# Kernel tuning notes

Measured on AMD Instinct MI355X. Metric: run time of the kernel, lower is better.

Reference implementation:

```python
import jax, jax.numpy as jnp
import numpy as np
import math

N_NODES = 16384
N_GRAPHS = 512
E2 = 65536
E3 = 393216
EMB = 300
SCH = 128
NG = 50
CUTOFF = 10.0
NL_GIN = 5
NL_SCH = 6
NTASK = 12


def _ssp(x):
    # ShiftedSoftplus used by SchNet
    return jax.nn.softplus(x) - math.log(2.0)


def _seg(x, ids, n):
    return jax.ops.segment_sum(x, ids, num_segments=n)


def _forward(x2d, edge_index_2d, edge_attr_2d, batch, z, pos, edge_index_3d,
             atom_emb1, atom_emb2, vn_init,
             gin_W1, gin_b1, gin_W2, gin_b2, gin_bond1, gin_bond2, gin_gamma, gin_beta,
             vn_W1, vn_b1, vn_W2, vn_b2,
             sch_emb, s_mW1, s_mb1, s_mW2, s_mb2, s_lin1W, s_lin2W, s_lin2b, s_linW, s_linb,
             p2W, p2b, p3W, p3b, gW1, gb1, gW2, gb2, cW1, cb1, cW2, cb2):
    counts = jnp.maximum(_seg(jnp.ones((N_NODES,), jnp.float32), batch, N_GRAPHS), 1.0)[:, None]
    # ---------- GIN (2D) encoder with virtual node (OGB-style, eval mode: dropout off, BN uses running stats 0/1) ----------
    src2, dst2 = edge_index_2d[0], edge_index_2d[1]
    h = atom_emb1[x2d[:, 0]] + atom_emb2[x2d[:, 1]]              # [N, 300]
    vn = jnp.broadcast_to(vn_init, (N_GRAPHS, EMB))
    for l in range(NL_GIN):
        h_in = h + vn[batch]
        eemb = gin_bond1[l][edge_attr_2d[:, 0]] + gin_bond2[l][edge_attr_2d[:, 1]]
        msg = jax.nn.relu(h_in[src2] + eemb)                     # [E2, 300]
        agg = _seg(msg, dst2, N_NODES)
        t = jax.nn.relu((h_in + agg) @ gin_W1[l] + gin_b1[l]) @ gin_W2[l] + gin_b2[l]
        t = t * gin_gamma[l] + gin_beta[l]                       # eval-mode BatchNorm
        if l < NL_GIN - 1:
            t = jax.nn.relu(t)
            vn_tmp = _seg(t, batch, N_GRAPHS) + vn
            vn = jax.nn.relu(jax.nn.relu(vn_tmp @ vn_W1[l] + vn_b1[l]) @ vn_W2[l] + vn_b2[l])
        h = t
    h2d = _seg(h, batch, N_GRAPHS) / counts                      # global_mean_pool
    # ---------- SchNet (3D) encoder: interaction layers only, residual additions ----------
    src3, dst3 = edge_index_3d[0], edge_index_3d[1]
    diff = pos[dst3] - pos[src3]
    d = jnp.sqrt(jnp.sum(diff * diff, axis=-1))                  # edge_weight [E3]; no self loops -> d > 0
    offsets = jnp.linspace(0.0, CUTOFF, NG)
    coeff = -0.5 / (offsets[1] - offsets[0]) ** 2
    rbf = jnp.exp(coeff * (d[:, None] - offsets) ** 2)           # GaussianSmearing [E3, 50]
    C = 0.5 * (jnp.cos(d * math.pi / CUTOFF) + 1.0)              # cosine cutoff
    hs = sch_emb[z]                                              # [N, 128]
    for l in range(NL_SCH):
        Wf = (_ssp(rbf @ s_mW1[l] + s_mb1[l]) @ s_mW2[l] + s_mb2[l]) * C[:, None]  # filter net [E3, 128]
        x1 = hs @ s_lin1W[l]                                     # CFConv lin1 (no bias)
        agg = _seg(x1[src3] * Wf, dst3, N_NODES)                 # continuous-filter conv
        x2 = agg @ s_lin2W[l] + s_lin2b[l]                       # CFConv lin2
        hs = hs + (_ssp(x2) @ s_linW[l] + s_linb[l])             # block act+lin, residual
    h3d = _seg(hs, batch, N_GRAPHS) / counts
    # ---------- gated fusion + classifier (dropout off in eval) ----------
    h2p = h2d @ p2W + p2b
    h3p = h3d @ p3W + p3b
    g = jax.nn.sigmoid(jax.nn.relu(jnp.concatenate([h2p, h3p], axis=1) @ gW1 + gb1) @ gW2 + gb2)  # [B, 1]
    hf = g * h2p + (1.0 - g) * h3p
    return jax.nn.relu(hf @ cW1 + cb1) @ cW2 + cb2               # [N_GRAPHS, NTASK]


def setup_inputs() -> dict:
    key = jax.random.key(0)
    ks = jax.random.split(key, 40)
    def r(i, shape, s=0.02):
        return jax.random.normal(ks[i], shape, dtype=jnp.float32) * s
    x2d = jax.random.randint(ks[0], (N_NODES, 2), 0, 3)
    src2 = jax.random.randint(ks[1], (E2,), 0, N_NODES)
    dst2 = (src2 + jax.random.randint(ks[2], (E2,), 1, N_NODES)) % N_NODES  # no self loops
    edge_index_2d = jnp.stack([src2, dst2])
    edge_attr_2d = jax.random.randint(ks[3], (E2, 2), 0, 3)
    batch = jnp.sort(jax.random.randint(ks[4], (N_NODES,), 0, N_GRAPHS))
    z = jax.random.randint(ks[5], (N_NODES,), 0, 100)
    pos = jax.random.normal(ks[6], (N_NODES, 3), dtype=jnp.float32) * 2.0
    src3 = jax.random.randint(ks[7], (E3,), 0, N_NODES)
    dst3 = (src3 + jax.random.randint(ks[8], (E3,), 1, N_NODES)) % N_NODES
    edge_index_3d = jnp.stack([src3, dst3])
    return dict(
        x2d=x2d, edge_index_2d=edge_index_2d, edge_attr_2d=edge_attr_2d, batch=batch,
        z=z, pos=pos, edge_index_3d=edge_index_3d,
        atom_emb1=r(9, (120, EMB)), atom_emb2=r(10, (3, EMB)),
        vn_init=jnp.zeros((EMB,), jnp.float32),
        gin_W1=r(11, (NL_GIN, EMB, 2 * EMB)), gin_b1=jnp.zeros((NL_GIN, 2 * EMB), jnp.float32),
        gin_W2=r(12, (NL_GIN, 2 * EMB, EMB)), gin_b2=jnp.zeros((NL_GIN, EMB), jnp.float32),
        gin_bond1=r(13, (NL_GIN, 6, EMB)), gin_bond2=r(14, (NL_GIN, 3, EMB)),
        gin_gamma=jnp.ones((NL_GIN, EMB), jnp.float32), gin_beta=jnp.zeros((NL_GIN, EMB), jnp.float32),
        vn_W1=r(15, (NL_GIN - 1, EMB, 2 * EMB)), vn_b1=jnp.zeros((NL_GIN - 1, 2 * EMB), jnp.float32),
        vn_W2=r(16, (NL_GIN - 1, 2 * EMB, EMB)), vn_b2=jnp.zeros((NL_GIN - 1, EMB), jnp.float32),
        sch_emb=r(17, (100, SCH), 0.1),
        s_mW1=r(18, (NL_SCH, NG, SCH), 0.1), s_mb1=jnp.zeros((NL_SCH, SCH), jnp.float32),
        s_mW2=r(19, (NL_SCH, SCH, SCH), 0.1), s_mb2=jnp.zeros((NL_SCH, SCH), jnp.float32),
        s_lin1W=r(20, (NL_SCH, SCH, SCH), 0.1),
        s_lin2W=r(21, (NL_SCH, SCH, SCH), 0.1), s_lin2b=jnp.zeros((NL_SCH, SCH), jnp.float32),
        s_linW=r(22, (NL_SCH, SCH, SCH), 0.1), s_linb=jnp.zeros((NL_SCH, SCH), jnp.float32),
        p2W=r(23, (EMB, EMB)), p2b=jnp.zeros((EMB,), jnp.float32),
        p3W=r(24, (SCH, EMB)), p3b=jnp.zeros((EMB,), jnp.float32),
        gW1=r(25, (2 * EMB, 128)), gb1=jnp.zeros((128,), jnp.float32),
        gW2=r(26, (128, 1)), gb2=jnp.zeros((1,), jnp.float32),
        cW1=r(27, (EMB, EMB // 2)), cb1=jnp.zeros((EMB // 2,), jnp.float32),
        cW2=r(28, (EMB // 2, NTASK)), cb2=jnp.zeros((NTASK,), jnp.float32),
    )


def reference(x2d, edge_index_2d, edge_attr_2d, batch, z, pos, edge_index_3d,
              atom_emb1, atom_emb2, vn_init,
              gin_W1, gin_b1, gin_W2, gin_b2, gin_bond1, gin_bond2, gin_gamma, gin_beta,
              vn_W1, vn_b1, vn_W2, vn_b2,
              sch_emb, s_mW1, s_mb1, s_mW2, s_mb2, s_lin1W, s_lin2W, s_lin2b, s_linW, s_linb,
              p2W, p2b, p3W, p3b, gW1, gb1, gW2, gb2, cW1, cb1, cW2, cb2):
    return _forward(x2d, edge_index_2d, edge_attr_2d, batch, z, pos, edge_index_3d,
                    atom_emb1, atom_emb2, vn_init,
                    gin_W1, gin_b1, gin_W2, gin_b2, gin_bond1, gin_bond2, gin_gamma, gin_beta,
                    vn_W1, vn_b1, vn_W2, vn_b2,
                    sch_emb, s_mW1, s_mb1, s_mW2, s_mb2, s_lin1W, s_lin2W, s_lin2b, s_linW, s_linb,
                    p2W, p2b, p3W, p3b, gW1, gb1, gW2, gb2, cW1, cb1, cW2, cb2)
```

## Files before the change

### kernel.cpp

```cpp
#include <hip/hip_runtime.h>
#include <hip/hip_bf16.h>
#include <math.h>

#define NN 16384
#define NG 512
#define NE2 65536
#define NE3 393216
#define DEMB 300
#define DSCH 128
#define NRBF 50
#define NTAB 5120
#define TROWS 5121
#define DMAX 25.0f

typedef __attribute__((ext_vector_type(8))) short bf16x8;
typedef __attribute__((ext_vector_type(4))) float f32x4;

__device__ __forceinline__ float sspf(float x) {
  float sp = log1pf(expf(-fabsf(x))) + fmaxf(x, 0.f);
  return sp - 0.69314718055994530942f;
}

__device__ __forceinline__ short f2b(float f) {
  union { float f; unsigned u; } v;
  v.f = f;
  unsigned r = v.u + 0x7FFF + ((v.u >> 16) & 1);
  return (short)(r >> 16);
}

__device__ __forceinline__ float b2f(unsigned short b) {
  union { unsigned u; float f; } v;
  v.u = ((unsigned)b) << 16;
  return v.f;
}


__global__ void k_hist3(const int* __restrict__ ei2, const int* __restrict__ ei3,
                        const int* __restrict__ batch, int* __restrict__ cnt2,
                        int* __restrict__ cnt3, int* __restrict__ cntg) {
  int i = blockIdx.x * blockDim.x + threadIdx.x;
  if (i < NE2) {
    atomicAdd(&cnt2[ei2[NE2 + i]], 1);
  } else if (i < NE2 + NE3) {
    atomicAdd(&cnt3[ei3[NE3 + (i - NE2)]], 1);
  } else if (i < NE2 + NE3 + NN) {
    atomicAdd(&cntg[batch[i - NE2 - NE3]], 1);
  }
}

__global__ __launch_bounds__(1024) void k_scan3(const int* __restrict__ c0, int* __restrict__ o0,
                                                int n0, const int* __restrict__ c1,
                                                int* __restrict__ o1, int n1,
                                                const int* __restrict__ c2, int* __restrict__ o2,
                                                int n2) {
  const int* cnt = (blockIdx.x == 0) ? c0 : (blockIdx.x == 1) ? c1 : c2;
  int* off = (blockIdx.x == 0) ? o0 : (blockIdx.x == 1) ? o1 : o2;
  int n = (blockIdx.x == 0) ? n0 : (blockIdx.x == 1) ? n1 : n2;
  __shared__ int part[1024];
  int tid = threadIdx.x;
  int per = (n + 1023) / 1024;
  int base = tid * per;
  int sum = 0;
  for (int i = 0; i < per; ++i) {
    int idx = base + i;
    if (idx < n) sum += cnt[idx];
  }
  part[tid] = sum;
  __syncthreads();
  for (int d = 1; d < 1024; d <<= 1) {
    int v = (tid >= d) ? part[tid - d] : 0;
    __syncthreads();
    part[tid] += v;
    __syncthreads();
  }
  int run = (tid == 0) ? 0 : part[tid - 1];
  for (int i = 0; i < per; ++i) {
    int idx = base + i;
    if (idx < n) {
      off[idx] = run;
      run += cnt[idx];
    }
  }
  if (tid == 0) off[n] = part[1023];
}

__global__ void k_scatterB(const int* __restrict__ ei2, const int* __restrict__ ea2,
                           const int* __restrict__ batch, const int* __restrict__ off2,
                           int* __restrict__ cur2, int* __restrict__ s2s, int* __restrict__ ec2s,
                           int* __restrict__ b2s, const int* __restrict__ ei3,
                           const float* __restrict__ pos, const int* __restrict__ off3,
                           int* __restrict__ cur3, int* __restrict__ s3s, int* __restrict__ id3s,
                           float* __restrict__ fr3s) {
  int i = blockIdx.x * blockDim.x + threadIdx.x;
  if (i < NE2) {
    int e = i;
    int s = ei2[e], d = ei2[NE2 + e];
    int p = atomicAdd(&cur2[d], 1);
    int j = off2[d] + p;
    s2s[j] = s;
    ec2s[j] = ea2[2 * e] * 4 + ea2[2 * e + 1];
    b2s[j] = batch[s];
  } else if (i < NE2 + NE3) {
    int e = i - NE2;
    int s = ei3[e], d = ei3[NE3 + e];
    float dx = pos[3 * d] - pos[3 * s];
    float dy = pos[3 * d + 1] - pos[3 * s + 1];
    float dz = pos[3 * d + 2] - pos[3 * s + 2];
    float dist = sqrtf(dx * dx + dy * dy + dz * dz);
    float u = fminf(dist * ((float)NTAB / DMAX), (float)NTAB - 0.001f);
    int idx = (int)u;
    int p = atomicAdd(&cur3[d], 1);
    int j = off3[d] + p;
    s3s[j] = s;
    id3s[j] = idx;
    fr3s[j] = u - (float)idx;
  }
}


__global__ void k_init_gin(const int* __restrict__ x2d, const float* __restrict__ e1,
                           const float* __restrict__ e2, short* __restrict__ hb,
                           const float* __restrict__ vni, float* __restrict__ vn,
                           short* __restrict__ vnb) {
  int i = blockIdx.x * blockDim.x + threadIdx.x;
  if (i < NN * DEMB) {
    int n = i / DEMB, c = i - n * DEMB;
    hb[i] = f2b(e1[x2d[2 * n] * DEMB + c] + e2[x2d[2 * n + 1] * DEMB + c]);
  } else if (i < NN * DEMB + NG * DEMB) {
    int j = i - NN * DEMB;
    float v = vni[j % DEMB];
    vn[j] = v;
    vnb[j] = f2b(v);
  }
}

__global__ void k_init_sch(float* __restrict__ rbs, float* __restrict__ Cs,
                           const int* __restrict__ z, const float* __restrict__ emb,
                           float* __restrict__ hs, short* __restrict__ hsb) {
  int i = blockIdx.x * blockDim.x + threadIdx.x;
  if (i < TROWS * NRBF) {
    int j = i / NRBF, k = i - j * NRBF;
    float dj = (float)j * (DMAX / (float)NTAB);
    const float step = 10.0f / 49.0f;
    const float coeff = -0.5f / (step * step);
    float t = dj - (float)k * step;
    rbs[i] = expf(coeff * t * t);
    if (k == 0) Cs[j] = 0.5f * (cosf(dj * (3.14159265358979323846f / 10.0f)) + 1.0f);
  } else if (i < TROWS * NRBF + NN * DSCH) {
    int j = i - TROWS * NRBF;
    float v = emb[z[j >> 7] * DSCH + (j & 127)];
    hs[j] = v;
    hsb[j] = f2b(v);
  }
}

__global__ __launch_bounds__(256) void k_head4(
    const float* __restrict__ h2d, const float* __restrict__ h3d, const float* __restrict__ p2W,
    const float* __restrict__ p2b, const float* __restrict__ p3W, const float* __restrict__ p3b,
    const float* __restrict__ gW1, const float* __restrict__ gb1, const float* __restrict__ gW2,
    const float* __restrict__ gb2, const float* __restrict__ cW1, const float* __restrict__ cb1,
    const float* __restrict__ cW2, const float* __restrict__ cb2, float* __restrict__ out) {
  __shared__ float sx[DEMB], sy[DSCH], h2p[DEMB], h3p[DEMB], ghl[DSCH], c1l[150];
  __shared__ float pa[2][128], pb[2][128];
  __shared__ float gshare;
  int g = blockIdx.x, tid = threadIdx.x;
  int half = tid >> 7, o7 = tid & 127;
  for (int i = tid; i < DEMB; i += 256) sx[i] = h2d[(size_t)g * DEMB + i];
  if (tid < DSCH) sy[tid] = h3d[(size_t)g * DSCH + tid];
  __syncthreads();
  for (int ob = 0; ob < DEMB; ob += 128) {
    int o = ob + o7;
    float a = 0.f, b = 0.f;
    if (o < DEMB) {
      for (int k = half * 150; k < half * 150 + 150; ++k) a = fmaf(sx[k], p2W[k * 300 + o], a);
      for (int k = half * 64; k < half * 64 + 64; ++k) b = fmaf(sy[k], p3W[k * 300 + o], b);
    }
    pa[half][o7] = a;
    pb[half][o7] = b;
    __syncthreads();
    if (half == 0 && o < DEMB) {
      h2p[o] = pa[0][o7] + pa[1][o7] + p2b[o];
      h3p[o] = pb[0][o7] + pb[1][o7] + p3b[o];
    }
    __syncthreads();
  }
  {
    float a = 0.f;
    if (half == 0) {
      for (int k = 0; k < 300; ++k) a = fmaf(h2p[k], gW1[k * 128 + o7], a);
    } else {
      for (int k = 0; k < 300; ++k) a = fmaf(h3p[k], gW1[(300 + k) * 128 + o7], a);
    }
    pa[half][o7] = a;
    __syncthreads();
    if (half == 0) ghl[o7] = fmaxf(pa[0][o7] + pa[1][o7] + gb1[o7], 0.f);
    __syncthreads();
  }
  if (tid < 128) pa[0][tid] = ghl[tid] * gW2[tid];
  __syncthreads();
  for (int s = 64; s > 0; s >>= 1) {
    if (tid < s) pa[0][tid] += pa[0][tid + s];
    __syncthreads();
  }
  if (tid == 0) gshare = 1.0f / (1.0f + expf(-(pa[0][0] + gb2[0])));
  __syncthreads();
  float gg = gshare;
  for (int i = tid; i < DEMB; i += 256) sx[i] = gg * h2p[i] + (1.0f - gg) * h3p[i];
  __syncthreads();
  for (int ob = 0; ob < 150; ob += 128) {
    int o = ob + o7;
    float a = 0.f;
    if (o < 150) {
      for (int k = half * 150; k < half * 150 + 150; ++k) a = fmaf(sx[k], cW1[k * 150 + o], a);
    }
    pa[half][o7] = a;
    __syncthreads();
    if (half == 0 && o < 150) c1l[o] = fmaxf(pa[0][o7] + pa[1][o7] + cb1[o], 0.f);
    __syncthreads();
  }
  if (tid < 12) {
    float a = cb2[tid];
    for (int k = 0; k < 150; ++k) a = fmaf(c1l[k], cW2[k * 12 + tid], a);
    out[(size_t)g * 12 + tid] = a;
  }
}


__global__ __launch_bounds__(256) void k_gin_gather4(
    const short* __restrict__ hb, const short* __restrict__ vnb, const int* __restrict__ batch,
    const int* __restrict__ off2, const int* __restrict__ s2s, const int* __restrict__ ec2s,
    const int* __restrict__ b2s, const float* __restrict__ bond1,
    const float* __restrict__ bond2, short* __restrict__ aggb) {
  __shared__ float sb[9 * DEMB];
  int tid = threadIdx.x;
  for (int i = tid; i < 6 * DEMB; i += 256) sb[i] = bond1[i];
  for (int i = tid; i < 3 * DEMB; i += 256) sb[6 * DEMB + i] = bond2[i];
  __syncthreads();
  int d = blockIdx.x * 4 + (tid >> 6);
  int lane = tid & 63;
  int j0 = off2[d], j1 = off2[d + 1];
  const unsigned short* hd = (const unsigned short*)hb + (size_t)d * DEMB;
  const unsigned short* vd = (const unsigned short*)vnb + (size_t)batch[d] * DEMB;
  float acc[5];
#pragma unroll
  for (int q = 0; q < 5; ++q) {
    int col = lane + 64 * q;
    acc[q] = (col < DEMB) ? b2f(hd[col]) + b2f(vd[col]) : 0.f;
  }
  for (int j = j0; j < j1; ++j) {
    int s = s2s[j], ec = ec2s[j], bs = b2s[j];
    const unsigned short* hr = (const unsigned short*)hb + (size_t)s * DEMB;
    const unsigned short* vr = (const unsigned short*)vnb + (size_t)bs * DEMB;
    const float* b1 = sb + (ec >> 2) * DEMB;
    const float* b2 = sb + 6 * DEMB + (ec & 3) * DEMB;
#pragma unroll
    for (int q = 0; q < 5; ++q) {
      int col = lane + 64 * q;
      if (col < DEMB) acc[q] += fmaxf(b2f(hr[col]) + b2f(vr[col]) + b1[col] + b2[col], 0.f);
    }
  }
  short* outr = aggb + (size_t)d * 320;
#pragma unroll
  for (int q = 0; q < 5; ++q) {
    int col = lane + 64 * q;
    outr[col] = (col < DEMB) ? f2b(acc[q]) : (short)0;
  }
}

__global__ __launch_bounds__(256) void k_conv_gather4(
    const short* __restrict__ ftabb, const short* __restrict__ x1b, const int* __restrict__ off3,
    const int* __restrict__ s3s, const int* __restrict__ id3s, const float* __restrict__ fr3s,
    short* __restrict__ agg3b) {
  int tid = threadIdx.x;
  int d = blockIdx.x * 4 + (tid >> 6);
  int lane = tid & 63;
  int j0 = off3[d], j1 = off3[d + 1];
  float a0 = 0.f, a1 = 0.f;
  for (int j = j0; j < j1; ++j) {
    int s = s3s[j], idx = id3s[j];
    float fr = fr3s[j];
    unsigned t0 = ((const unsigned*)(ftabb + (size_t)idx * 128))[lane];
    unsigned t1 = ((const unsigned*)(ftabb + (size_t)(idx + 1) * 128))[lane];
    unsigned xv = ((const unsigned*)(x1b + (size_t)s * 128))[lane];
    float t0a = b2f((unsigned short)(t0 & 0xFFFF)), t0b = b2f((unsigned short)(t0 >> 16));
    float t1a = b2f((unsigned short)(t1 & 0xFFFF)), t1b = b2f((unsigned short)(t1 >> 16));
    a0 += (t0a + fr * (t1a - t0a)) * b2f((unsigned short)(xv & 0xFFFF));
    a1 += (t0b + fr * (t1b - t0b)) * b2f((unsigned short)(xv >> 16));
  }
  unsigned pack = ((unsigned)(unsigned short)f2b(a1) << 16) | (unsigned short)f2b(a0);
  ((unsigned*)(agg3b + (size_t)d * 128))[lane] = pack;
}

__global__ __launch_bounds__(256) void k_poolb300(const short* __restrict__ xb,
                                                  const int* __restrict__ goff,
                                                  float* __restrict__ out) {
  int g = blockIdx.x * 4 + (threadIdx.x >> 6);
  int lane = threadIdx.x & 63;
  if (g >= NG) return;
  int r0 = goff[g], r1 = goff[g + 1];
  float acc[5] = {};
  for (int r = r0; r < r1; ++r) {
    const unsigned short* row = (const unsigned short*)xb + (size_t)r * DEMB;
#pragma unroll
    for (int q = 0; q < 5; ++q) {
      int col = lane + 64 * q;
      if (col < DEMB) acc[q] += b2f(row[col]);
    }
  }
  float s = 1.0f / fmaxf((float)(r1 - r0), 1.0f);
#pragma unroll
  for (int q = 0; q < 5; ++q) {
    int col = lane + 64 * q;
    if (col < DEMB) out[(size_t)g * DEMB + col] = acc[q] * s;
  }
}

__global__ __launch_bounds__(256) void k_poolb128(const short* __restrict__ xb,
                                                  const int* __restrict__ goff,
                                                  float* __restrict__ out) {
  int g = blockIdx.x * 4 + (threadIdx.x >> 6);
  int lane = threadIdx.x & 63;
  if (g >= NG) return;
  int r0 = goff[g], r1 = goff[g + 1];
  float a0 = 0.f, a1 = 0.f;
  for (int r = r0; r < r1; ++r) {
    unsigned v = ((const unsigned*)(xb + (size_t)r * DSCH))[lane];
    a0 += b2f((unsigned short)(v & 0xFFFF));
    a1 += b2f((unsigned short)(v >> 16));
  }
  float s = 1.0f / fmaxf((float)(r1 - r0), 1.0f);
  out[(size_t)g * DSCH + lane * 2] = a0 * s;
  out[(size_t)g * DSCH + lane * 2 + 1] = a1 * s;
}

__global__ __launch_bounds__(256) void k_poolvn(const short* __restrict__ hb,
                                                const int* __restrict__ goff,
                                                const float* __restrict__ vn,
                                                short* __restrict__ vnab) {
  int g = blockIdx.x * 4 + (threadIdx.x >> 6);
  int lane = threadIdx.x & 63;
  if (g >= NG) return;
  int r0 = goff[g], r1 = goff[g + 1];
  float acc[5] = {};
  for (int r = r0; r < r1; ++r) {
    const unsigned short* row = (const unsigned short*)hb + (size_t)r * DEMB;
#pragma unroll
    for (int q = 0; q < 5; ++q) {
      int col = lane + 64 * q;
      if (col < DEMB) acc[q] += b2f(row[col]);
    }
  }
  short* outr = vnab + (size_t)g * 320;
#pragma unroll
  for (int q = 0; q < 5; ++q) {
    int col = lane + 64 * q;
    if (col < 320)
      outr[col] = (col < DEMB) ? f2b(acc[q] + vn[(size_t)g * DEMB + col]) : (short)0;
  }
}

__global__ void k_prepw2(const float* __restrict__ Wa, const float* __restrict__ Wb,
                         short* __restrict__ Wta, short* __restrict__ Wtb, int K, int N, int Kp,
                         int Np, int La, int Lb) {
  int i = blockIdx.x * blockDim.x + threadIdx.x;
  int per = Np * Kp;
  if (i >= (La + Lb) * per) return;
  int l = i / per, r = i - l * per;
  int n = r / Kp, k = r - n * Kp;
  const float* W = (l < La) ? Wa : Wb;
  int ll = (l < La) ? l : l - La;
  short* Wt = (l < La) ? Wta : Wtb;
  float v = (n < N && k < K) ? W[(size_t)ll * K * N + (size_t)k * N + n] : 0.f;
  Wt[(size_t)ll * per + r] = f2b(v);
}

__global__ void k_prepw3(const float* __restrict__ W0, const float* __restrict__ W1,
                         const float* __restrict__ W2, short* __restrict__ T0,
                         short* __restrict__ T1, short* __restrict__ T2) {
  int i = blockIdx.x * blockDim.x + threadIdx.x;
  const int per = 6 * 128 * 128;
  if (i >= 3 * per) return;
  int which = i / per, r = i - which * per;
  int l = r / 16384, rr = r - l * 16384;
  int n = rr / 128, k = rr - n * 128;
  const float* W = (which == 0) ? W0 : (which == 1) ? W1 : W2;
  short* T = (which == 0) ? T0 : (which == 1) ? T1 : T2;
  T[r] = f2b(W[(size_t)l * 16384 + (size_t)k * 128 + n]);
}

template <int ACT>
__global__ __launch_bounds__(256) void k_gemmz(
    const float* __restrict__ A, const float* __restrict__ B, const float* __restrict__ bias,
    const float* __restrict__ rscale, float* __restrict__ Cout, short* __restrict__ Coutb,
    int M, int N, int K, int ldc, long strideA, long strideB, long strideBias, long strideC) {
  A += (size_t)blockIdx.z * strideA;
  B += (size_t)blockIdx.z * strideB;
  bias += (size_t)blockIdx.z * strideBias;
  __shared__ float sA[16][65];
  __shared__ float sB[16][64];
  int tid = threadIdx.x;
  int tx = tid & 15, ty = tid >> 4;
  int bm = blockIdx.y * 64, bn = blockIdx.x * 64;
  float acc[4][4] = {};
  for (int k0 = 0; k0 < K; k0 += 16) {
#pragma unroll
    for (int t = 0; t < 4; ++t) {
      int i = tid + t * 256;
      int m = i >> 4, kk = i & 15;
      int gm = bm + m, gk = k0 + kk;
      sA[kk][m] = (gm < M && gk < K) ? A[(size_t)gm * K + gk] : 0.f;
    }
#pragma unroll
    for (int t = 0; t < 4; ++t) {
      int i = tid + t * 256;
      int kk = i >> 6, n = i & 63;
      int gk = k0 + kk, gn = bn + n;
      sB[kk][n] = (gk < K && gn < N) ? B[(size_t)gk * N + gn] : 0.f;
    }
    __syncthreads();
#pragma unroll
    for (int kk = 0; kk < 16; ++kk) {
      float a[4], b[4];
#pragma unroll
      for (int i = 0; i < 4; ++i) a[i] = sA[kk][ty + 16 * i];
#pragma unroll
      for (int j = 0; j < 4; ++j) b[j] = sB[kk][tx + 16 * j];
#pragma unroll
      for (int i = 0; i < 4; ++i)
#pragma unroll
        for (int j = 0; j < 4; ++j) acc[i][j] = fmaf(a[i], b[j], acc[i][j]);
    }
    __syncthreads();
  }
#pragma unroll
  for (int i = 0; i < 4; ++i) {
    int gm = bm + ty + 16 * i;
    if (gm >= M) continue;
    float rs = rscale ? rscale[gm] : 1.0f;
#pragma unroll
    for (int j = 0; j < 4; ++j) {
      int gn = bn + tx + 16 * j;
      if (gn >= N) continue;
      float v = acc[i][j] + bias[gn];
      if (ACT == 1) v = fmaxf(v, 0.f);
      if (ACT == 2) v = sspf(v);
      v *= rs;
      if (Cout) Cout[(size_t)blockIdx.z * strideC + (size_t)gm * ldc + gn] = v;
      if (Coutb) Coutb[(size_t)blockIdx.z * strideC + (size_t)gm * ldc + gn] = f2b(v);
    }
  }
}

template <int ACT>
__global__ __launch_bounds__(256) void k_mgemm_bf(
    const short* __restrict__ Ab, const short* __restrict__ Wt, const float* __restrict__ bias,
    const float* __restrict__ scale, const float* __restrict__ shift,
    const float* __restrict__ Cin, float* __restrict__ Cout, short* __restrict__ Coutb,
    int M, int N, int Kp, int ldc, int ldcb, int Nb) {
  __shared__ short sA[128 * 32];
  const int tid = threadIdx.x;
  const int lane = tid & 63;
  const int w = tid >> 6;
  const int wm = w >> 1, wn = w & 1;
  const int bm = blockIdx.y * 128, bn = blockIdx.x * 128;

  f32x4 acc[4][4] = {};

  const int sr = tid >> 1;
  const int sk = (tid & 1) * 16;
  const short* Arow = Ab + (size_t)(bm + sr) * Kp + sk;
  const int ssw = (sr + (sr >> 2)) & 3;
  const int s0 = (sk >> 3);
  bf16x8* sAv = (bf16x8*)sA;

  const int frow = wm * 64 + (lane & 15);
  const int fslot = lane >> 4;
  const short* Bbase = Wt + (size_t)(bn + wn * 64 + (lane & 15)) * Kp + (fslot * 8);

  for (int k0 = 0; k0 < Kp; k0 += 32) {
    __syncthreads();
    {
      bf16x8 p0 = *(const bf16x8*)(Arow + k0);
      bf16x8 p1 = *(const bf16x8*)(Arow + k0 + 8);
      sAv[sr * 4 + ((s0 + 0) ^ ssw)] = p0;
      sAv[sr * 4 + ((s0 + 1) ^ ssw)] = p1;
    }
    __syncthreads();

    bf16x8 af[4], bfr[4];
#pragma unroll
    for (int mf = 0; mf < 4; ++mf) {
      int r = frow + mf * 16;
      af[mf] = sAv[r * 4 + (fslot ^ ((r + (r >> 2)) & 3))];
    }
#pragma unroll
    for (int nf = 0; nf < 4; ++nf) bfr[nf] = *(const bf16x8*)(Bbase + (size_t)nf * 16 * Kp + k0);
#pragma unroll
    for (int mf = 0; mf < 4; ++mf)
#pragma unroll
      for (int nf = 0; nf < 4; ++nf)
        acc[mf][nf] =
            __builtin_amdgcn_mfma_f32_16x16x32_bf16(af[mf], bfr[nf], acc[mf][nf], 0, 0, 0);
  }

  const int colbase = bn + wn * 64 + (lane & 15);
  const int rowbase = bm + wm * 64 + ((lane >> 4) << 2);
#pragma unroll
  for (int nf = 0; nf < 4; ++nf) {
    int col = colbase + nf * 16;
    bool cv = col < N;
    float bi = (bias && cv) ? bias[col] : 0.f;
    float sc = (scale && cv) ? scale[col] : 1.f;
    float sh = (shift && cv) ? shift[col] : 0.f;
#pragma unroll
    for (int mf = 0; mf < 4; ++mf) {
      f32x4 v = acc[mf][nf];
#pragma unroll
      for (int j = 0; j < 4; ++j) {
        int row = rowbase + mf * 16 + j;
        float x = v[j] + bi;
        if (scale) x = x * sc + sh;
        if (ACT == 1) x = fmaxf(x, 0.f);
        if (ACT == 2) x = sspf(x);
        if (Cin && cv) x += Cin[(size_t)row * ldc + col];
        if (Cout && cv) Cout[(size_t)row * ldc + col] = x;
        if (Coutb && col < Nb) Coutb[(size_t)row * ldcb + col] = cv ? f2b(x) : (short)0;
      }
    }
  }
}

template <int ACT>
__global__ __launch_bounds__(256) void k_mgemm_bf64(
    const short* __restrict__ Ab, const short* __restrict__ Wt, const float* __restrict__ bias,
    const float* __restrict__ scale, const float* __restrict__ shift,
    const float* __restrict__ Cin, float* __restrict__ Cout, short* __restrict__ Coutb,
    int M, int N, int Kp, int ldc, int ldcb, int Nb) {
  __shared__ short sA[64 * 32];
  const int tid = threadIdx.x;
  const int lane = tid & 63;
  const int w = tid >> 6;
  const int bm = blockIdx.y * 64, bn = blockIdx.x * 128;

  f32x4 acc[4][2] = {};

  const int sr = tid >> 2;
  const int sk = (tid & 3) * 8;
  const short* Arow = Ab + (size_t)(bm + sr) * Kp + sk;
  const int ssw = (sr + (sr >> 2)) & 3;
  const int s0 = tid & 3;
  bf16x8* sAv = (bf16x8*)sA;

  const int frow = lane & 15;
  const int fslot = lane >> 4;
  const short* Bbase = Wt + (size_t)(bn + w * 32 + (lane & 15)) * Kp + (fslot * 8);

  for (int k0 = 0; k0 < Kp; k0 += 32) {
    __syncthreads();
    sAv[sr * 4 + (s0 ^ ssw)] = *(const bf16x8*)(Arow + k0);
    __syncthreads();

    bf16x8 af[4], bfr[2];
#pragma unroll
    for (int mf = 0; mf < 4; ++mf) {
      int r = frow + mf * 16;
      af[mf] = sAv[r * 4 + (fslot ^ ((r + (r >> 2)) & 3))];
    }
#pragma unroll
    for (int nf = 0; nf < 2; ++nf) bfr[nf] = *(const bf16x8*)(Bbase + (size_t)nf * 16 * Kp + k0);
#pragma unroll
    for (int mf = 0; mf < 4; ++mf)
#pragma unroll
      for (int nf = 0; nf < 2; ++nf)
        acc[mf][nf] =
            __builtin_amdgcn_mfma_f32_16x16x32_bf16(af[mf], bfr[nf], acc[mf][nf], 0, 0, 0);
  }

  const int colbase = bn + w * 32 + (lane & 15);
  const int rowbase = bm + ((lane >> 4) << 2);
#pragma unroll
  for (int nf = 0; nf < 2; ++nf) {
    int col = colbase + nf * 16;
    bool cv = col < N;
    float bi = (bias && cv) ? bias[col] : 0.f;
    float sc = (scale && cv) ? scale[col] : 1.f;
    float sh = (shift && cv) ? shift[col] : 0.f;
#pragma unroll
    for (int mf = 0; mf < 4; ++mf) {
      f32x4 v = acc[mf][nf];
#pragma unroll
      for (int j = 0; j < 4; ++j) {
        int row = rowbase + mf * 16 + j;
        float x = v[j] + bi;
        if (scale) x = x * sc + sh;
        if (ACT == 1) x = fmaxf(x, 0.f);
        if (ACT == 2) x = sspf(x);
        if (Cin && cv) x += Cin[(size_t)row * ldc + col];
        if (Cout && cv) Cout[(size_t)row * ldc + col] = x;
        if (Coutb && col < Nb) Coutb[(size_t)row * ldcb + col] = cv ? f2b(x) : (short)0;
      }
    }
  }
}


static inline void run_mgemm_bf(hipStream_t st, const short* Ab, const short* Wt,
                                const float* bias, const float* scale, const float* shift,
                                const float* Cin, float* Cout, short* Coutb, int M, int N, int Kp,
                                int ldc, int ldcb, int Nb, int act) {
  dim3 grid((N + 127) / 128, M / 128);
  if (act == 0)
    k_mgemm_bf<0><<<grid, 256, 0, st>>>(Ab, Wt, bias, scale, shift, Cin, Cout, Coutb, M, N, Kp,
                                        ldc, ldcb, Nb);
  else if (act == 1)
    k_mgemm_bf<1><<<grid, 256, 0, st>>>(Ab, Wt, bias, scale, shift, Cin, Cout, Coutb, M, N, Kp,
                                        ldc, ldcb, Nb);
  else
    k_mgemm_bf<2><<<grid, 256, 0, st>>>(Ab, Wt, bias, scale, shift, Cin, Cout, Coutb, M, N, Kp,
                                        ldc, ldcb, Nb);
}

static inline void run_mgemm_bf64(hipStream_t st, const short* Ab, const short* Wt,
                                  const float* bias, const float* scale, const float* shift,
                                  const float* Cin, float* Cout, short* Coutb, int M, int N,
                                  int Kp, int ldc, int ldcb, int Nb, int act) {
  dim3 grid((N + 127) / 128, M / 64);
  if (act == 0)
    k_mgemm_bf64<0><<<grid, 256, 0, st>>>(Ab, Wt, bias, scale, shift, Cin, Cout, Coutb, M, N, Kp,
                                          ldc, ldcb, Nb);
  else if (act == 1)
    k_mgemm_bf64<1><<<grid, 256, 0, st>>>(Ab, Wt, bias, scale, shift, Cin, Cout, Coutb, M, N, Kp,
                                          ldc, ldcb, Nb);
  else
    k_mgemm_bf64<2><<<grid, 256, 0, st>>>(Ab, Wt, bias, scale, shift, Cin, Cout, Coutb, M, N, Kp,
                                          ldc, ldcb, Nb);
}

extern "C" void kernel_launch(void* const* d_in, const int* in_sizes, int n_in, void* d_out,
                              int out_size, void* d_ws, size_t ws_size, hipStream_t stream) {
  const int* x2d = (const int*)d_in[0];
  const int* ei2 = (const int*)d_in[1];
  const int* ea2 = (const int*)d_in[2];
  const int* batch = (const int*)d_in[3];
  const int* z = (const int*)d_in[4];
  const float* pos = (const float*)d_in[5];
  const int* ei3 = (const int*)d_in[6];
  const float* atom_emb1 = (const float*)d_in[7];
  const float* atom_emb2 = (const float*)d_in[8];
  const float* vn_init = (const float*)d_in[9];
  const float* gin_W1 = (const float*)d_in[10];
  const float* gin_b1 = (const float*)d_in[11];
  const float* gin_W2 = (const float*)d_in[12];
  const float* gin_b2 = (const float*)d_in[13];
  const float* gin_bond1 = (const float*)d_in[14];
  const float* gin_bond2 = (const float*)d_in[15];
  const float* gin_gamma = (const float*)d_in[16];
  const float* gin_beta = (const float*)d_in[17];
  const float* vn_W1 = (const float*)d_in[18];
  const float* vn_b1 = (const float*)d_in[19];
  const float* vn_W2 = (const float*)d_in[20];
  const float* vn_b2 = (const float*)d_in[21];
  const float* sch_emb = (const float*)d_in[22];
  const float* s_mW1 = (const float*)d_in[23];
  const float* s_mb1 = (const float*)d_in[24];
  const float* s_mW2 = (const float*)d_in[25];
  const float* s_mb2 = (const float*)d_in[26];
  const float* s_lin1W = (const float*)d_in[27];
  const float* s_lin2W = (const float*)d_in[28];
  const float* s_lin2b = (const float*)d_in[29];
  const float* s_linW = (const float*)d_in[30];
  const float* s_linb = (const float*)d_in[31];
  const float* p2W = (const float*)d_in[32];
  const float* p2b = (const float*)d_in[33];
  const float* p3W = (const float*)d_in[34];
  const float* p3b = (const float*)d_in[35];
  const float* gW1 = (const float*)d_in[36];
  const float* gb1 = (const float*)d_in[37];
  const float* gW2 = (const float*)d_in[38];
  const float* gb2 = (const float*)d_in[39];
  const float* cW1 = (const float*)d_in[40];
  const float* cb1 = (const float*)d_in[41];
  const float* cW2 = (const float*)d_in[42];
  const float* cb2 = (const float*)d_in[43];

  float* ws = (float*)d_ws;
  short* hb = (short*)ws;
  int* b2s = (int*)(ws + 2500000);
  short* aggb = (short*)(ws + 5000000);
  short* y1b = (short*)(ws + 7700000);
  float* rbs = ws + 400000;
  float* Cs = ws + 700000;
  float* t1all = ws + 800000;
  short* ftabb = (short*)(ws + 4800000);
  float* hs = ws + 8800000;
  short* x1b = (short*)(ws + 11000000);
  short* agg3b = (short*)(ws + 13200000);
  short* hsb = (short*)(ws + 15400000);
  short* W1t = (short*)(ws + 20000000);
  short* W2t = (short*)(ws + 20600000);
  short* s1t = (short*)(ws + 21200000);
  short* s2t = (short*)(ws + 21300000);
  short* s3t = (short*)(ws + 21400000);
  int* I = (int*)(ws + 22000000);
  int* cnt2 = I + 0;
  int* cnt3 = I + 16384;
  int* cntg = I + 32768;
  int* cur2 = I + 33280;
  int* cur3 = I + 49664;
  int* off2 = I + 70000;
  int* off3 = I + 90000;
  int* goff = I + 110000;
  int* s2s = I + 120000;
  int* ec2s = I + 190000;
  int* s3s = I + 260000;
  int* id3s = I + 660000;
  float* fr3s = (float*)(I + 1060000);
  short* vnW1t = (short*)(ws + 23500000);
  short* vnW2t = (short*)(ws + 24000000);
  short* vnab = (short*)(ws + 24500000);
  short* vnhb = (short*)(ws + 24600000);
  short* vnb = (short*)(ws + 24800000);
  float* vn = ws + 28443136;
  float* h2d = ws + 29057536;
  float* h3d = ws + 29211136;

  k_prepw2<<<(9 * 640 * 320 + 255) / 256, 256, 0, stream>>>(gin_W1, vn_W1, W1t, vnW1t, 300, 600,
                                                            320, 640, 5, 4);
  k_prepw2<<<(9 * 384 * 608 + 255) / 256, 256, 0, stream>>>(gin_W2, vn_W2, W2t, vnW2t, 600, 300,
                                                            608, 384, 5, 4);
  k_prepw3<<<(3 * 6 * 16384 + 255) / 256, 256, 0, stream>>>(s_lin1W, s_lin2W, s_linW, s1t, s2t,
                                                            s3t);

  hipMemsetAsync(I, 0, 66048 * sizeof(int), stream);
  k_hist3<<<(NE2 + NE3 + NN + 255) / 256, 256, 0, stream>>>(ei2, ei3, batch, cnt2, cnt3, cntg);
  k_scan3<<<3, 1024, 0, stream>>>(cnt2, off2, 16384, cnt3, off3, 16384, cntg, goff, 512);
  k_scatterB<<<(NE2 + NE3 + 255) / 256, 256, 0, stream>>>(ei2, ea2, batch, off2, cur2, s2s, ec2s,
                                                          b2s, ei3, pos, off3, cur3, s3s, id3s,
                                                          fr3s);

  k_init_gin<<<(NN * DEMB + NG * DEMB + 255) / 256, 256, 0, stream>>>(x2d, atom_emb1, atom_emb2,
                                                                      hb, vn_init, vn, vnb);
  for (int l = 0; l < 5; ++l) {
    k_gin_gather4<<<NN / 4, 256, 0, stream>>>(hb, vnb, batch, off2, s2s, ec2s, b2s,
                                              gin_bond1 + l * 6 * DEMB, gin_bond2 + l * 3 * DEMB,
                                              aggb);
    run_mgemm_bf(stream, aggb, W1t + (size_t)l * 640 * 320, gin_b1 + l * 600, nullptr, nullptr,
                 nullptr, nullptr, y1b, NN, 600, 320, 0, 608, 608, 1);
    run_mgemm_bf(stream, y1b, W2t + (size_t)l * 384 * 608, gin_b2 + l * 300, gin_gamma + l * 300,
                 gin_beta + l * 300, nullptr, nullptr, hb, NN, 300, 608, 0, 300, 300,
                 (l < 4) ? 1 : 0);
    if (l < 4) {
      k_poolvn<<<NG / 4, 256, 0, stream>>>(hb, goff, vn, vnab);
      run_mgemm_bf64(stream, vnab, vnW1t + (size_t)l * 640 * 320, vn_b1 + l * 600, nullptr,
                     nullptr, nullptr, nullptr, vnhb, NG, 600, 320, 0, 608, 608, 1);
      run_mgemm_bf64(stream, vnhb, vnW2t + (size_t)l * 384 * 608, vn_b2 + l * 300, nullptr,
                     nullptr, nullptr, vn, vnb, NG, 300, 608, 300, 300, 300, 1);
    }
  }
  k_poolb300<<<NG / 4, 256, 0, stream>>>(hb, goff, h2d);

  k_init_sch<<<(TROWS * NRBF + NN * DSCH + 255) / 256, 256, 0, stream>>>(rbs, Cs, z, sch_emb, hs,
                                                                         hsb);
  {
    dim3 ga(2, (TROWS + 63) / 64, 6);
    k_gemmz<2><<<ga, 256, 0, stream>>>(rbs, s_mW1, s_mb1, nullptr, t1all, nullptr, TROWS, 128, 50,
                                       128, 0L, 50L * 128, 128L, (long)TROWS * 128);
    k_gemmz<0><<<ga, 256, 0, stream>>>(t1all, s_mW2, s_mb2, Cs, nullptr, ftabb, TROWS, 128, 128,
                                       128, (long)TROWS * 128, 128L * 128, 128L,
                                       (long)TROWS * 128);
  }
  for (int l = 0; l < 6; ++l) {
    run_mgemm_bf64(stream, hsb, s1t + (size_t)l * 16384, nullptr, nullptr, nullptr, nullptr,
                   nullptr, x1b, NN, 128, 128, 0, 128, 128, 0);
    k_conv_gather4<<<NN / 4, 256, 0, stream>>>(ftabb + (size_t)l * TROWS * 128, x1b, off3, s3s,
                                               id3s, fr3s, agg3b);
    run_mgemm_bf64(stream, agg3b, s2t + (size_t)l * 16384, s_lin2b + l * 128, nullptr, nullptr,
                   nullptr, nullptr, x1b, NN, 128, 128, 0, 128, 128, 2);
    run_mgemm_bf64(stream, x1b, s3t + (size_t)l * 16384, s_linb + l * 128, nullptr, nullptr, hs,
                   hs, hsb, NN, 128, 128, 128, 128, 128, 0);
  }
  k_poolb128<<<NG / 4, 256, 0, stream>>>(hsb, goff, h3d);

  k_head4<<<NG, 256, 0, stream>>>(h2d, h3d, p2W, p2b, p3W, p3b, gW1, gb1, gW2, gb2, cW1, cb1, cW2,
                                  cb2, (float*)d_out);
}
```

Before: 1.439 ms.

## Fuse SchNet interaction GEMM chain into one kernel and split head accumulators

Measured after the change: 1.349 ms. 1.07x faster.

```diff
diff --git a/kernel.cpp b/kernel.cpp
--- a/kernel.cpp
+++ b/kernel.cpp
@@ -154,7 +154,7 @@
   }
 }
 
-__global__ __launch_bounds__(256) void k_head4(
+__global__ __launch_bounds__(256) void k_head5(
     const float* __restrict__ h2d, const float* __restrict__ h3d, const float* __restrict__ p2W,
     const float* __restrict__ p2b, const float* __restrict__ p3W, const float* __restrict__ p3b,
     const float* __restrict__ gW1, const float* __restrict__ gb1, const float* __restrict__ gW2,
@@ -170,13 +170,21 @@
   __syncthreads();
   for (int ob = 0; ob < DEMB; ob += 128) {
     int o = ob + o7;
-    float a = 0.f, b = 0.f;
+    float a0 = 0.f, a1 = 0.f, b0 = 0.f, b1 = 0.f;
     if (o < DEMB) {
-      for (int k = half * 150; k < half * 150 + 150; ++k) a = fmaf(sx[k], p2W[k * 300 + o], a);
-      for (int k = half * 64; k < half * 64 + 64; ++k) b = fmaf(sy[k], p3W[k * 300 + o], b);
-    }
-    pa[half][o7] = a;
-    pb[half][o7] = b;
+      int kb = half * 150;
+      for (int k = kb; k < kb + 150; k += 2) {
+        a0 = fmaf(sx[k], p2W[k * 300 + o], a0);
+        a1 = fmaf(sx[k + 1], p2W[(k + 1) * 300 + o], a1);
+      }
+      int kb3 = half * 64;
+      for (int k = kb3; k < kb3 + 64; k += 2) {
+        b0 = fmaf(sy[k], p3W[k * 300 + o], b0);
+        b1 = fmaf(sy[k + 1], p3W[(k + 1) * 300 + o], b1);
+      }
+    }
+    pa[half][o7] = a0 + a1;
+    pb[half][o7] = b0 + b1;
     __syncthreads();
     if (half == 0 && o < DEMB) {
       h2p[o] = pa[0][o7] + pa[1][o7] + p2b[o];
@@ -185,13 +193,16 @@
     __syncthreads();
   }
   {
-    float a = 0.f;
-    if (half == 0) {
-      for (int k = 0; k < 300; ++k) a = fmaf(h2p[k], gW1[k * 128 + o7], a);
-    } else {
-      for (int k = 0; k < 300; ++k) a = fmaf(h3p[k], gW1[(300 + k) * 128 + o7], a);
-    }
-    pa[half][o7] = a;
+    const float* src = (half == 0) ? h2p : h3p;
+    const float* wb = gW1 + (half ? 300 * 128 : 0);
+    float a0 = 0.f, a1 = 0.f, a2 = 0.f, a3 = 0.f;
+    for (int k = 0; k < 300; k += 4) {
+      a0 = fmaf(src[k], wb[k * 128 + o7], a0);
+      a1 = fmaf(src[k + 1], wb[(k + 1) * 128 + o7], a1);
+      a2 = fmaf(src[k + 2], wb[(k + 2) * 128 + o7], a2);
+      a3 = fmaf(src[k + 3], wb[(k + 3) * 128 + o7], a3);
+    }
+    pa[half][o7] = (a0 + a1) + (a2 + a3);
     __syncthreads();
     if (half == 0) ghl[o7] = fmaxf(pa[0][o7] + pa[1][o7] + gb1[o7], 0.f);
     __syncthreads();
@@ -209,11 +220,15 @@
   __syncthreads();
   for (int ob = 0; ob < 150; ob += 128) {
     int o = ob + o7;
-    float a = 0.f;
+    float a0 = 0.f, a1 = 0.f;
     if (o < 150) {
-      for (int k = half * 150; k < half * 150 + 150; ++k) a = fmaf(sx[k], cW1[k * 150 + o], a);
-    }
-    pa[half][o7] = a;
+      int kb = half * 150;
+      for (int k = kb; k < kb + 150; k += 2) {
+        a0 = fmaf(sx[k], cW1[k * 150 + o], a0);
+        a1 = fmaf(sx[k + 1], cW1[(k + 1) * 150 + o], a1);
+      }
+    }
+    pa[half][o7] = a0 + a1;
     __syncthreads();
     if (half == 0 && o < 150) c1l[o] = fmaxf(pa[0][o7] + pa[1][o7] + cb1[o], 0.f);
     __syncthreads();
@@ -599,6 +614,142 @@
         if (Cout && cv) Cout[(size_t)row * ldc + col] = x;
         if (Coutb && col < Nb) Coutb[(size_t)row * ldcb + col] = cv ? f2b(x) : (short)0;
       }
+    }
+  }
+}
+
+template <int LAST>
+__global__ __launch_bounds__(256) void k_sch_fused(
+    const short* __restrict__ agg3b, const short* __restrict__ W2t, const float* __restrict__ b2,
+    const short* __restrict__ W3t, const float* __restrict__ b3, const short* __restrict__ W1n,
+    float* __restrict__ hs, short* __restrict__ hsb, short* __restrict__ x1b) {
+  __shared__ short sA[64 * 128];
+  __shared__ short sY[64 * 128];
+  const int tid = threadIdx.x;
+  const int lane = tid & 63;
+  const int w = tid >> 6;
+  const int bm = blockIdx.x * 64;
+  bf16x8* sAv = (bf16x8*)sA;
+  bf16x8* sYv = (bf16x8*)sY;
+  {
+    int r = tid >> 2, q = tid & 3;
+    int ssw = (r + (r >> 2)) & 3;
+    const short* Arow = agg3b + (size_t)(bm + r) * 128 + q * 8;
+#pragma unroll
+    for (int c = 0; c < 4; ++c) sAv[r * 16 + c * 4 + (q ^ ssw)] = *(const bf16x8*)(Arow + c * 32);
+  }
+  __syncthreads();
+  const int frow = lane & 15;
+  const int fslot = lane >> 4;
+  const int colw = w * 32 + (lane & 15);
+  const int rw0 = (lane >> 4) << 2;
+  {
+    f32x4 acc[4][2] = {};
+    const short* Bbase = W2t + (size_t)colw * 128 + fslot * 8;
+#pragma unroll
+    for (int c = 0; c < 4; ++c) {
+      bf16x8 af[4], bfr[2];
+#pragma unroll
+      for (int mf = 0; mf < 4; ++mf) {
+        int r = frow + mf * 16;
+        af[mf] = sAv[r * 16 + c * 4 + (fslot ^ ((r + (r >> 2)) & 3))];
+      }
+#pragma unroll
+      for (int nf = 0; nf < 2; ++nf) bfr[nf] = *(const bf16x8*)(Bbase + nf * 16 * 128 + c * 32);
+#pragma unroll
+      for (int mf = 0; mf < 4; ++mf)
+#pragma unroll
+        for (int nf = 0; nf < 2; ++nf)
+          acc[mf][nf] =
+              __builtin_amdgcn_mfma_f32_16x16x32_bf16(af[mf], bfr[nf], acc[mf][nf], 0, 0, 0);
+    }
+#pragma unroll
+    for (int nf = 0; nf < 2; ++nf) {
+      int cl = colw + nf * 16;
+      float bi = b2[cl];
+#pragma unroll
+      for (int mf = 0; mf < 4; ++mf)
+#pragma unroll
+        for (int j = 0; j < 4; ++j) {
+          int rw = rw0 + mf * 16 + j;
+          float y = sspf(acc[mf][nf][j] + bi);
+          int slot = (cl >> 5) * 4 + (((cl >> 3) & 3) ^ ((rw + (rw >> 2)) & 3));
+          sY[rw * 128 + slot * 8 + (cl & 7)] = f2b(y);
+        }
+    }
+  }
+  __syncthreads();
+  {
+    f32x4 acc[4][2] = {};
+    const short* Bbase = W3t + (size_t)colw * 128 + fslot * 8;
+#pragma unroll
+    for (int c = 0; c < 4; ++c) {
+      bf16x8 af[4], bfr[2];
+#pragma unroll
+      for (int mf = 0; mf < 4; ++mf) {
+        int r = frow + mf * 16;
+        af[mf] = sYv[r * 16 + c * 4 + (fslot ^ ((r + (r >> 2)) & 3))];
+      }
+#pragma unroll
+      for (int nf = 0; nf < 2; ++nf) bfr[nf] = *(const bf16x8*)(Bbase + nf * 16 * 128 + c * 32);
+#pragma unroll
+      for (int mf = 0; mf < 4; ++mf)
+#pragma unroll
+        for (int nf = 0; nf < 2; ++nf)
+          acc[mf][nf] =
+              __builtin_amdgcn_mfma_f32_16x16x32_bf16(af[mf], bfr[nf], acc[mf][nf], 0, 0, 0);
+    }
+#pragma unroll
+    for (int nf = 0; nf < 2; ++nf) {
+      int cl = colw + nf * 16;
+      float bi = b3[cl];
+#pragma unroll
+      for (int mf = 0; mf < 4; ++mf)
+#pragma unroll
+        for (int j = 0; j < 4; ++j) {
+          int rw = rw0 + mf * 16 + j;
+          size_t gi = (size_t)(bm + rw) * 128 + cl;
+          float x = acc[mf][nf][j] + bi + hs[gi];
+          hs[gi] = x;
+          short xb = f2b(x);
+          hsb[gi] = xb;
+          int slot = (cl >> 5) * 4 + (((cl >> 3) & 3) ^ ((rw + (rw >> 2)) & 3));
+          sA[rw * 128 + slot * 8 + (cl & 7)] = xb;
+        }
+    }
+  }
+  if (LAST) return;
+  __syncthreads();
+  {
+    f32x4 acc[4][2] = {};
+    const short* Bbase = W1n + (size_t)colw * 128 + fslot * 8;
+#pragma unroll
+    for (int c = 0; c < 4; ++c) {
+      bf16x8 af[4], bfr[2];
+#pragma unroll
+      for (int mf = 0; mf < 4; ++mf) {
+        int r = frow + mf * 16;
+        af[mf] = sAv[r * 16 + c * 4 + (fslot ^ ((r + (r >> 2)) & 3))];
+      }
+#pragma unroll
+      for (int nf = 0; nf < 2; ++nf) bfr[nf] = *(const bf16x8*)(Bbase + nf * 16 * 128 + c * 32);
+#pragma unroll
+      for (int mf = 0; mf < 4; ++mf)
+#pragma unroll
+        for (int nf = 0; nf < 2; ++nf)
+          acc[mf][nf] =
+              __builtin_amdgcn_mfma_f32_16x16x32_bf16(af[mf], bfr[nf], acc[mf][nf], 0, 0, 0);
+    }
+#pragma unroll
+    for (int nf = 0; nf < 2; ++nf) {
+      int cl = colw + nf * 16;
+#pragma unroll
+      for (int mf = 0; mf < 4; ++mf)
+#pragma unroll
+        for (int j = 0; j < 4; ++j) {
+          int rw = rw0 + mf * 16 + j;
+          x1b[(size_t)(bm + rw) * 128 + cl] = f2b(acc[mf][nf][j]);
+        }
     }
   }
 }
@@ -769,18 +920,23 @@
                                        128, (long)TROWS * 128, 128L * 128, 128L,
                                        (long)TROWS * 128);
   }
+  run_mgemm_bf64(stream, hsb, s1t, nullptr, nullptr, nullptr, nullptr, nullptr, x1b, NN, 128, 128,
+                 0, 128, 128, 0);
   for (int l = 0; l < 6; ++l) {
-    run_mgemm_bf64(stream, hsb, s1t + (size_t)l * 16384, nullptr, nullptr, nullptr, nullptr,
-                   nullptr, x1b, NN, 128, 128, 0, 128, 128, 0);
     k_conv_gather4<<<NN / 4, 256, 0, stream>>>(ftabb + (size_t)l * TROWS * 128, x1b, off3, s3s,
                                                id3s, fr3s, agg3b);
-    run_mgemm_bf64(stream, agg3b, s2t + (size_t)l * 16384, s_lin2b + l * 128, nullptr, nullptr,
-                   nullptr, nullptr, x1b, NN, 128, 128, 0, 128, 128, 2);
-    run_mgemm_bf64(stream, x1b, s3t + (size_t)l * 16384, s_linb + l * 128, nullptr, nullptr, hs,
-                   hs, hsb, NN, 128, 128, 128, 128, 128, 0);
+    if (l < 5)
+      k_sch_fused<0><<<NN / 64, 256, 0, stream>>>(agg3b, s2t + (size_t)l * 16384,
+                                                  s_lin2b + l * 128, s3t + (size_t)l * 16384,
+                                                  s_linb + l * 128, s1t + (size_t)(l + 1) * 16384,
+                                                  hs, hsb, x1b);
+    else
+      k_sch_fused<1><<<NN / 64, 256, 0, stream>>>(agg3b, s2t + (size_t)l * 16384,
+                                                  s_lin2b + l * 128, s3t + (size_t)l * 16384,
+                                                  s_linb + l * 128, s1t, hs, hsb, x1b);
   }
   k_poolb128<<<NG / 4, 256, 0, stream>>>(hsb, goff, h3d);
 
-  k_head4<<<NG, 256, 0, stream>>>(h2d, h3d, p2W, p2b, p3W, p3b, gW1, gb1, gW2, gb2, cW1, cb1, cW2,
+  k_head5<<<NG, 256, 0, stream>>>(h2d, h3d, p2W, p2b, p3W, p3b, gW1, gb1, gW2, gb2, cW1, cb1, cW2,
                                   cb2, (float*)d_out);
 }
```
